# Kernel tuning notes

Measured on AMD Instinct MI355X. Metric: run time of the kernel, lower is better.

The kernel has to match this reference:

```python
import jax, jax.numpy as jnp
import numpy as np

D = 128      # state_dim
ED = 20      # edge_dim (RBF basis size)
R = 3        # num message/update rounds
G = 3        # gated equivariant blocks
CUT = 5.0    # cutoff
N = 10000    # nodes
E = 160000   # edges
B = 500      # molecules
HRO = 64     # readout hidden


def setup_inputs() -> dict:
    key = jax.random.key(0)
    ks = jax.random.split(key, 40)
    sc = 0.05

    def nrm(k, shape):
        return jax.random.normal(k, shape, dtype=jnp.float32) * sc

    inp = {
        "h": jax.random.normal(ks[0], (N, 5), dtype=jnp.float32),
        "pos": jax.random.normal(ks[1], (N, 3), dtype=jnp.float32),
        "edge_index": jax.random.randint(ks[2], (2, E), 0, N),
        "batch": jnp.sort(jax.random.randint(ks[3], (N,), 0, B)),
        # node embedding Linear(5, D)
        "emb_w": nrm(ks[4], (5, D)), "emb_b": nrm(ks[5], (D,)),
        # per-round message params (stacked over rounds)
        "msg_phi_w1": nrm(ks[6], (R, D, D)), "msg_phi_b1": nrm(ks[7], (R, D)),
        "msg_phi_w2": nrm(ks[8], (R, D, 3 * D)), "msg_phi_b2": nrm(ks[9], (R, 3 * D)),
        "msg_filt_w": nrm(ks[10], (R, ED, 3 * D)), "msg_filt_b": nrm(ks[11], (R, 3 * D)),
        # per-round update params
        "upd_U": nrm(ks[12], (R, D, D)), "upd_V": nrm(ks[13], (R, D, D)),
        "upd_w1": nrm(ks[14], (R, 2 * D, D)), "upd_b1": nrm(ks[15], (R, D)),
        "upd_w2": nrm(ks[16], (R, D, 3 * D)), "upd_b2": nrm(ks[17], (R, 3 * D)),
        # gated equivariant blocks
        "geb_wv1": nrm(ks[18], (G, D, D)), "geb_wv2": nrm(ks[19], (G, D, D)),
        "geb_w1": nrm(ks[20], (G, 2 * D, D)), "geb_b1": nrm(ks[21], (G, D)),
        "geb_w2": nrm(ks[22], (G, D, 2 * D)), "geb_b2": nrm(ks[23], (G, 2 * D)),
        # invariant readout MLP
        "ro_w1": nrm(ks[24], (D, HRO)), "ro_b1": nrm(ks[25], (HRO,)),
        "ro_w2": nrm(ks[26], (HRO, 1)), "ro_b2": nrm(ks[27], (1,)),
    }
    return inp


def _safe_norm(x, axis):
    return jnp.sqrt(jnp.sum(x * x, axis=axis) + 1e-8)


def reference(h, pos, edge_index, batch,
              emb_w, emb_b,
              msg_phi_w1, msg_phi_b1, msg_phi_w2, msg_phi_b2,
              msg_filt_w, msg_filt_b,
              upd_U, upd_V, upd_w1, upd_b1, upd_w2, upd_b2,
              geb_wv1, geb_wv2, geb_w1, geb_b1, geb_w2, geb_b2,
              ro_w1, ro_b1, ro_w2, ro_b2):
    n_nodes = h.shape[0]
    row, col = edge_index[0], edge_index[1]
    # edge vectors: r_ij = pos[col] - pos[row]
    r_ij = pos[col] - pos[row]                                   # [E,3]
    d = jnp.clip(jnp.linalg.norm(r_ij, axis=1, keepdims=True), 1e-6, None)  # [E,1]
    unit = r_ij / d                                              # [E,3]
    # sinc radial basis + cosine cutoff
    freqs = jnp.arange(1, ED + 1, dtype=h.dtype)
    rbf = jnp.sin(freqs * jnp.pi * d / CUT) / d                  # [E,ED]
    fcut = 0.5 * (jnp.cos(jnp.pi * d / CUT) + 1.0) * (d < CUT)   # [E,1]

    s = h @ emb_w + emb_b                                        # [N,D]
    v = jnp.zeros((n_nodes, D, 3), dtype=h.dtype)                # [N,D,3]

    for r in range(R):
        # --- PaiNNMessage ---
        phi = jax.nn.silu(s @ msg_phi_w1[r] + msg_phi_b1[r]) @ msg_phi_w2[r] + msg_phi_b2[r]  # [N,3D]
        filt = (rbf @ msg_filt_w[r] + msg_filt_b[r]) * fcut      # [E,3D]
        x = phi[col] * filt                                      # gather + modulate  [E,3D]
        xs, xvv, xvw = jnp.split(x, 3, axis=-1)                  # each [E,D]
        ds = jax.ops.segment_sum(xs, row, num_segments=n_nodes)  # [N,D]
        dv_e = xvv[:, :, None] * v[col] + xvw[:, :, None] * unit[:, None, :]  # [E,D,3]
        dv = jax.ops.segment_sum(dv_e, row, num_segments=n_nodes)             # [N,D,3]
        s = s + ds
        v = v + dv
        # --- PaiNNUpdate ---
        Uv = jnp.einsum('ndc,de->nec', v, upd_U[r])              # [N,D,3]
        Vv = jnp.einsum('ndc,de->nec', v, upd_V[r])              # [N,D,3]
        Vn = _safe_norm(Vv, axis=-1)                             # [N,D]
        a = jax.nn.silu(jnp.concatenate([s, Vn], axis=-1) @ upd_w1[r] + upd_b1[r]) @ upd_w2[r] + upd_b2[r]
        a_ss, a_sv, a_vv = jnp.split(a, 3, axis=-1)
        s = s + a_ss + a_sv * jnp.sum(Uv * Vv, axis=-1)
        v = v + a_vv[:, :, None] * Uv

    # --- GatedEquivariantBlocks ---
    for g in range(G):
        v1 = jnp.einsum('ndc,de->nec', v, geb_wv1[g])
        v2 = jnp.einsum('ndc,de->nec', v, geb_wv2[g])
        n2 = _safe_norm(v2, axis=-1)                             # [N,D]
        a = jax.nn.silu(jnp.concatenate([s, n2], axis=-1) @ geb_w1[g] + geb_b1[g]) @ geb_w2[g] + geb_b2[g]
        s_new, gate = jnp.split(a, 2, axis=-1)
        s = s_new
        v = gate[:, :, None] * v1

    # --- InvariantReadout + molwise scatter ---
    out = jax.nn.silu(s @ ro_w1 + ro_b1) @ ro_w2 + ro_b2         # [N,1]
    molwise = jax.ops.segment_sum(out, batch, num_segments=B)    # [B,1]
    return molwise.squeeze(-1)
```

## Files before the change

### kernel.cpp

```cpp
#include <hip/hip_runtime.h>

typedef __attribute__((ext_vector_type(4))) float f32x4;
typedef __attribute__((ext_vector_type(8))) short short8;

#define D 128
#define D3 384
#define SLD 256
#define EDIM 20
#define NR 3
#define NG 3
#define CUTOFF 5.0f
#define NNODES 10000
#define NEDGES 160000
#define NMOL 500
#define HROH 64
#define PI_F 3.14159265358979323846f

#define FBIAS 1
#define FSILU 2

static __device__ __forceinline__ float silu_f(float x) {
    return x / (1.0f + expf(-x));
}

static __device__ __forceinline__ ushort f2bf(float x) {
    uint u = __float_as_uint(x);
    uint r = (u + 0x7fffu + ((u >> 16) & 1u)) >> 16;
    return (ushort)r;
}
static __device__ __forceinline__ float bf2f(ushort h) {
    return __uint_as_float((uint)h << 16);
}

#define TLR 64
#define TLC 64
#define KC 32
#define APAD 40
#define BPAD 36

template <bool TWO>
__global__ __launch_bounds__(256) void gemm_t(
    const float* __restrict__ A, int lda, int zsA,
    const float* __restrict__ WA, const float* __restrict__ WB, int ldw,
    const float* __restrict__ bias,
    float* __restrict__ CA, float* __restrict__ CB, int ldc, int zsC,
    int N, int K, int flags)
{
    int coord, sel;
    if (TWO) { coord = blockIdx.z >> 1; sel = blockIdx.z & 1; }
    else     { coord = blockIdx.z;      sel = 0; }
    const float* W = (TWO && sel) ? WB : WA;
    float* C = ((TWO && sel) ? CB : CA) + (size_t)coord * zsC;
    A += (size_t)coord * zsA;

    const int n0 = blockIdx.x * TLR;
    const int m0 = blockIdx.y * TLC;
    __shared__ ushort Ah[TLR * APAD], Al[TLR * APAD];
    __shared__ ushort Bh[TLC * BPAD], Bl[TLC * BPAD];
    const int tid = threadIdx.x;
    const int arow = tid & 63;
    const int akq = (tid >> 6) * 4;
    const bool aok = (n0 + arow) < N;
    const float* Ar = A + (size_t)(n0 + arow) * lda;
    const int bk = tid >> 4;
    const int bm = (tid & 15) * 4;
    const float* Wp = W + m0 + bm;
    const int lane = tid & 63;
    const int wrow = (tid >> 6) * 16;
    const int fr = lane & 15;
    const int kg = lane >> 4;
    const ushort* aph = Ah + (wrow + fr) * APAD + kg * 8;
    const ushort* apl = Al + (wrow + fr) * APAD + kg * 8;

    f32x4 acc[4];
    #pragma unroll
    for (int t = 0; t < 4; ++t) acc[t] = (f32x4){0.f, 0.f, 0.f, 0.f};

    for (int k0 = 0; k0 < K; k0 += KC) {
        #pragma unroll
        for (int half = 0; half < 2; ++half) {
            int kk = akq + half * 16;
            float4 v = aok ? *(const float4*)(Ar + k0 + kk)
                           : make_float4(0.f, 0.f, 0.f, 0.f);
            ushort h0 = f2bf(v.x), h1 = f2bf(v.y), h2 = f2bf(v.z), h3 = f2bf(v.w);
            ushort l0 = f2bf(v.x - bf2f(h0)), l1 = f2bf(v.y - bf2f(h1));
            ushort l2 = f2bf(v.z - bf2f(h2)), l3 = f2bf(v.w - bf2f(h3));
            uint2 ph, pl;
            ph.x = (uint)h0 | ((uint)h1 << 16); ph.y = (uint)h2 | ((uint)h3 << 16);
            pl.x = (uint)l0 | ((uint)l1 << 16); pl.y = (uint)l2 | ((uint)l3 << 16);
            *(uint2*)(Ah + arow * APAD + kk) = ph;
            *(uint2*)(Al + arow * APAD + kk) = pl;
        }
        #pragma unroll
        for (int half = 0; half < 2; ++half) {
            int kk = bk + half * 16;
            float4 v = *(const float4*)(Wp + (size_t)(k0 + kk) * ldw);
            float vv[4] = {v.x, v.y, v.z, v.w};
            #pragma unroll
            for (int i = 0; i < 4; ++i) {
                ushort hh = f2bf(vv[i]);
                ushort ll = f2bf(vv[i] - bf2f(hh));
                Bh[(bm + i) * BPAD + kk] = hh;
                Bl[(bm + i) * BPAD + kk] = ll;
            }
        }
        __syncthreads();
        short8 ah = *(const short8*)aph;
        short8 al = *(const short8*)apl;
        #pragma unroll
        for (int t = 0; t < 4; ++t) {
            const ushort* bp = Bh + (t * 16 + fr) * BPAD + kg * 8;
            const ushort* bq = Bl + (t * 16 + fr) * BPAD + kg * 8;
            short8 bh, bl;
            ((uint2*)&bh)[0] = *(const uint2*)bp;
            ((uint2*)&bh)[1] = *(const uint2*)(bp + 4);
            ((uint2*)&bl)[0] = *(const uint2*)bq;
            ((uint2*)&bl)[1] = *(const uint2*)(bq + 4);
            acc[t] = __builtin_amdgcn_mfma_f32_16x16x32_bf16(ah, bh, acc[t], 0, 0, 0);
            acc[t] = __builtin_amdgcn_mfma_f32_16x16x32_bf16(al, bh, acc[t], 0, 0, 0);
            acc[t] = __builtin_amdgcn_mfma_f32_16x16x32_bf16(ah, bl, acc[t], 0, 0, 0);
        }
        __syncthreads();
    }
    #pragma unroll
    for (int t = 0; t < 4; ++t) {
        #pragma unroll
        for (int r = 0; r < 4; ++r) {
            int n = n0 + wrow + kg * 4 + r;
            if (n < N) {
                int m = m0 + t * 16 + fr;
                float val = acc[t][r];
                float* cp = C + (size_t)n * ldc + m;
                if (flags & FBIAS) val += bias[m];
                if (flags & FSILU) val = silu_f(val);
                *cp = val;
            }
        }
    }
}

__global__ __launch_bounds__(256) void emb_k(
    const float* __restrict__ h, const float* __restrict__ w,
    const float* __restrict__ b, float* __restrict__ s, int total)
{
    int i = blockIdx.x * 256 + threadIdx.x;
    if (i >= total) return;
    int n = i >> 7, d = i & 127;
    float acc = b[d];
    #pragma unroll
    for (int k = 0; k < 5; ++k) acc = fmaf(h[n * 5 + k], w[k * D + d], acc);
    s[(size_t)n * SLD + d] = acc;
}

__global__ __launch_bounds__(256) void hist_k(const int* __restrict__ ei,
                                              int* __restrict__ cnt, int E)
{
    int e = blockIdx.x * 256 + threadIdx.x;
    if (e < E) atomicAdd(&cnt[ei[e]], 1);
}

__global__ __launch_bounds__(256) void scan_k(const int* __restrict__ cnt,
                                              int* __restrict__ offs, int n)
{
    __shared__ int tmp[256];
    __shared__ int carry;
    if (threadIdx.x == 0) carry = 0;
    __syncthreads();
    for (int base = 0; base < n; base += 256) {
        int i = base + threadIdx.x;
        int v = (i < n) ? cnt[i] : 0;
        tmp[threadIdx.x] = v;
        __syncthreads();
        for (int off = 1; off < 256; off <<= 1) {
            int add = (threadIdx.x >= off) ? tmp[threadIdx.x - off] : 0;
            __syncthreads();
            tmp[threadIdx.x] += add;
            __syncthreads();
        }
        if (i < n) offs[i + 1] = carry + tmp[threadIdx.x];
        __syncthreads();
        if (threadIdx.x == 255) carry += tmp[255];
        __syncthreads();
    }
    if (threadIdx.x == 0) offs[0] = 0;
}

__global__ __launch_bounds__(256) void initnext_k(const int* __restrict__ offs,
                                                  int* __restrict__ next, int n)
{
    int i = blockIdx.x * 256 + threadIdx.x;
    if (i < n) next[i] = offs[i];
}

__global__ __launch_bounds__(256) void edge_pre_k(
    const int* __restrict__ ei, const float* __restrict__ pos,
    int* __restrict__ next, float* __restrict__ rbf_s,
    float* __restrict__ uf_s, int* __restrict__ col_s, int E)
{
    int e = blockIdx.x * 256 + threadIdx.x;
    if (e >= E) return;
    int r = ei[e], c = ei[E + e];
    float dx = pos[c * 3 + 0] - pos[r * 3 + 0];
    float dy = pos[c * 3 + 1] - pos[r * 3 + 1];
    float dz = pos[c * 3 + 2] - pos[r * 3 + 2];
    float dist = sqrtf(dx * dx + dy * dy + dz * dz);
    float d = fmaxf(dist, 1e-6f);
    float inv = 1.0f / d;
    int p = atomicAdd(&next[r], 1);
    col_s[p] = c;
    uf_s[p * 4 + 0] = dx * inv;
    uf_s[p * 4 + 1] = dy * inv;
    uf_s[p * 4 + 2] = dz * inv;
    uf_s[p * 4 + 3] = (d < CUTOFF) ? 0.5f * (cosf(PI_F * d / CUTOFF) + 1.0f) : 0.0f;
    float w = PI_F * d / CUTOFF;
    #pragma unroll
    for (int k = 1; k <= EDIM; ++k)
        rbf_s[(size_t)p * EDIM + (k - 1)] = sinf((float)k * w) * inv;
}

#define MSG_NPB 4
__global__ __launch_bounds__(256) void message_csr_k(
    const int* __restrict__ offs, const int* __restrict__ col_s,
    const float* __restrict__ rbf_s, const float* __restrict__ uf_s,
    const float* __restrict__ P, const float* __restrict__ Vold,
    const float* __restrict__ Wf, const float* __restrict__ bf,
    float* __restrict__ S, float* __restrict__ Vnew, int N)
{
    const int sub = threadIdx.x >> 7;
    const int d = threadIdx.x & 127;
    float ws[EDIM], wvv[EDIM], wvw[EDIM];
    #pragma unroll
    for (int k = 0; k < EDIM; ++k) {
        ws[k]  = Wf[k * D3 + d];
        wvv[k] = Wf[k * D3 + D + d];
        wvw[k] = Wf[k * D3 + 2 * D + d];
    }
    const float bs = bf[d], bvv = bf[D + d], bvw = bf[2 * D + d];

    auto edge = [&](int j, float& ds, float& dvx, float& dvy, float& dvz) {
        float4 u4 = *(const float4*)(uf_s + (size_t)j * 4);
        int col = col_s[j];
        const float* rb = rbf_s + (size_t)j * EDIM;
        float4 r0 = *(const float4*)(rb);
        float4 r1 = *(const float4*)(rb + 4);
        float4 r2 = *(const float4*)(rb + 8);
        float4 r3 = *(const float4*)(rb + 12);
        float4 r4 = *(const float4*)(rb + 16);
        float rv[EDIM] = {r0.x, r0.y, r0.z, r0.w, r1.x, r1.y, r1.z, r1.w,
                          r2.x, r2.y, r2.z, r2.w, r3.x, r3.y, r3.z, r3.w,
                          r4.x, r4.y, r4.z, r4.w};
        float fs = bs, fvv = bvv, fvw = bvw;
        #pragma unroll
        for (int k = 0; k < EDIM; ++k) {
            fs  = fmaf(rv[k], ws[k], fs);
            fvv = fmaf(rv[k], wvv[k], fvv);
            fvw = fmaf(rv[k], wvw[k], fvw);
        }
        float fc = u4.w;
        const float* pc = P + (size_t)col * D3;
        const float* vc = Vold + (size_t)col * D3;
        float xs  = pc[d] * fs * fc;
        float xvv = pc[D + d] * fvv * fc;
        float xvw = pc[2 * D + d] * fvw * fc;
        ds += xs;
        dvx = fmaf(xvv, vc[d],         fmaf(xvw, u4.x, dvx));
        dvy = fmaf(xvv, vc[D + d],     fmaf(xvw, u4.y, dvy));
        dvz = fmaf(xvv, vc[2 * D + d], fmaf(xvw, u4.z, dvz));
    };

    for (int it = 0; it < MSG_NPB / 2; ++it) {
        int n = blockIdx.x * MSG_NPB + it * 2 + sub;
        if (n >= N) return;
        float ds0 = 0.f, dx0 = 0.f, dy0 = 0.f, dz0 = 0.f;
        float ds1 = 0.f, dx1 = 0.f, dy1 = 0.f, dz1 = 0.f;
        const int j0 = offs[n], j1 = offs[n + 1];
        int j = j0;
        for (; j + 2 <= j1; j += 2) {
            edge(j, ds0, dx0, dy0, dz0);
            edge(j + 1, ds1, dx1, dy1, dz1);
        }
        if (j < j1) edge(j, ds0, dx0, dy0, dz0);
        S[(size_t)n * SLD + d] += ds0 + ds1;
        const float* vo = Vold + (size_t)n * D3;
        float* vn = Vnew + (size_t)n * D3;
        vn[d]         = vo[d] + dx0 + dx1;
        vn[D + d]     = vo[D + d] + dy0 + dy1;
        vn[2 * D + d] = vo[2 * D + d] + dz0 + dz1;
    }
}

__global__ __launch_bounds__(256) void norm3_k(const float* __restrict__ V3,
                                               float* __restrict__ SX, int total)
{
    int i = blockIdx.x * 256 + threadIdx.x;
    if (i >= total) return;
    int n = i >> 7, d = i & 127;
    const float* b = V3 + (size_t)n * D3;
    float x = b[d], y = b[D + d], z = b[2 * D + d];
    SX[(size_t)n * SLD + D + d] = sqrtf(fmaf(x, x, fmaf(y, y, fmaf(z, z, 1e-8f))));
}

__global__ __launch_bounds__(256) void upd_apply_k(
    const float* __restrict__ U3, const float* __restrict__ V3,
    const float* __restrict__ P, float* __restrict__ s,
    float* __restrict__ v, int total)
{
    int i = blockIdx.x * 256 + threadIdx.x;
    if (i >= total) return;
    int n = i >> 7, d = i & 127;
    const float* u = U3 + (size_t)n * D3;
    const float* w = V3 + (size_t)n * D3;
    float ux = u[d], uy = u[D + d], uz = u[2 * D + d];
    float vx = w[d], vy = w[D + d], vz = w[2 * D + d];
    float dot = fmaf(ux, vx, fmaf(uy, vy, uz * vz));
    const float* a = P + (size_t)n * D3;
    s[(size_t)n * SLD + d] += a[d] + a[D + d] * dot;
    float avv = a[2 * D + d];
    float* vv = v + (size_t)n * D3;
    vv[d]         = fmaf(avv, ux, vv[d]);
    vv[D + d]     = fmaf(avv, uy, vv[D + d]);
    vv[2 * D + d] = fmaf(avv, uz, vv[2 * D + d]);
}

__global__ __launch_bounds__(256) void geb_apply_k(
    const float* __restrict__ P, const float* __restrict__ U3,
    float* __restrict__ s, float* __restrict__ v, int total)
{
    int i = blockIdx.x * 256 + threadIdx.x;
    if (i >= total) return;
    int n = i >> 7, d = i & 127;
    const float* a = P + (size_t)n * 2 * D;
    s[(size_t)n * SLD + d] = a[d];
    float g = a[D + d];
    const float* u = U3 + (size_t)n * D3;
    float* vv = v + (size_t)n * D3;
    vv[d]         = g * u[d];
    vv[D + d]     = g * u[D + d];
    vv[2 * D + d] = g * u[2 * D + d];
}

__global__ __launch_bounds__(256) void readout_k(
    const float* __restrict__ H2, const float* __restrict__ w2,
    const float* __restrict__ b2, const int* __restrict__ batch,
    float* __restrict__ out, int N)
{
    int n = blockIdx.x * 256 + threadIdx.x;
    if (n >= N) return;
    float acc = b2[0];
    const float* hrow = H2 + (size_t)n * HROH;
    #pragma unroll
    for (int k = 0; k < HROH; ++k) acc = fmaf(hrow[k], w2[k], acc);
    atomicAdd(out + batch[n], acc);
}


static inline void gemm(hipStream_t st, const float* A, int lda, int zsA,
                        const float* W, int ldw, const float* bias,
                        float* C, int ldc, int zsC,
                        int N, int K, int M, int flags, int Z = 1)
{
    dim3 g((N + TLR - 1) / TLR, M / TLC, Z);
    hipLaunchKernelGGL(HIP_KERNEL_NAME(gemm_t<false>), g, dim3(256), 0, st,
                       A, lda, zsA, W, nullptr, ldw, bias, C, nullptr, ldc, zsC,
                       N, K, flags);
}

static inline void gemm2(hipStream_t st, const float* A, int lda, int zsA,
                         const float* WA, const float* WB, int ldw,
                         float* CA, float* CB, int ldc, int zsC,
                         int N, int K, int M)
{
    dim3 g((N + TLR - 1) / TLR, M / TLC, 6);
    hipLaunchKernelGGL(HIP_KERNEL_NAME(gemm_t<true>), g, dim3(256), 0, st,
                       A, lda, zsA, WA, WB, ldw, nullptr, CA, CB, ldc, zsC,
                       N, K, 0);
}

extern "C" void kernel_launch(void* const* d_in, const int* in_sizes, int n_in,
                              void* d_out, int out_size, void* d_ws, size_t ws_size,
                              hipStream_t stream)
{
    const float* h          = (const float*)d_in[0];
    const float* pos        = (const float*)d_in[1];
    const int*   ei         = (const int*)d_in[2];
    const int*   batch      = (const int*)d_in[3];
    const float* emb_w      = (const float*)d_in[4];
    const float* emb_b      = (const float*)d_in[5];
    const float* msg_phi_w1 = (const float*)d_in[6];
    const float* msg_phi_b1 = (const float*)d_in[7];
    const float* msg_phi_w2 = (const float*)d_in[8];
    const float* msg_phi_b2 = (const float*)d_in[9];
    const float* msg_filt_w = (const float*)d_in[10];
    const float* msg_filt_b = (const float*)d_in[11];
    const float* upd_U      = (const float*)d_in[12];
    const float* upd_V      = (const float*)d_in[13];
    const float* upd_w1     = (const float*)d_in[14];
    const float* upd_b1     = (const float*)d_in[15];
    const float* upd_w2     = (const float*)d_in[16];
    const float* upd_b2     = (const float*)d_in[17];
    const float* geb_wv1    = (const float*)d_in[18];
    const float* geb_wv2    = (const float*)d_in[19];
    const float* geb_w1     = (const float*)d_in[20];
    const float* geb_b1     = (const float*)d_in[21];
    const float* geb_w2     = (const float*)d_in[22];
    const float* geb_b2     = (const float*)d_in[23];
    const float* ro_w1      = (const float*)d_in[24];
    const float* ro_b1      = (const float*)d_in[25];
    const float* ro_w2      = (const float*)d_in[26];
    const float* ro_b2      = (const float*)d_in[27];
    float* out = (float*)d_out;

    const int N = NNODES, E = NEDGES;

    char* p = (char*)d_ws;
    auto carve = [&](size_t bytes) {
        char* r = p;
        p += (bytes + 255) & ~(size_t)255;
        return r;
    };
    float* SX   = (float*)carve((size_t)N * SLD * 4);
    float* VA   = (float*)carve((size_t)N * D3 * 4);
    float* VB   = (float*)carve((size_t)N * D3 * 4);
    float* P_   = (float*)carve((size_t)N * D3 * 4);
    float* H    = (float*)carve((size_t)N * D * 4);
    float* H2   = (float*)carve((size_t)N * D * 4);
    float* V3   = (float*)carve((size_t)N * D3 * 4);
    float* RBFs = (float*)carve((size_t)E * EDIM * 4);
    float* UFs  = (float*)carve((size_t)E * 4 * 4);
    int*   COLs = (int*)carve((size_t)E * 4);
    int*   offs = (int*)carve((size_t)(N + 1) * 4);
    int*   nxt  = (int*)carve((size_t)N * 4);

    hipMemsetAsync(VA, 0, (size_t)N * D3 * 4, stream);
    hipLaunchKernelGGL(emb_k, dim3((N * D + 255) / 256), dim3(256), 0, stream,
                       h, emb_w, emb_b, SX, N * D);
    hipMemsetAsync(nxt, 0, (size_t)N * 4, stream);
    hipLaunchKernelGGL(hist_k, dim3((E + 255) / 256), dim3(256), 0, stream, ei, nxt, E);
    hipLaunchKernelGGL(scan_k, dim3(1), dim3(256), 0, stream, nxt, offs, N);
    hipLaunchKernelGGL(initnext_k, dim3((N + 255) / 256), dim3(256), 0, stream,
                       offs, nxt, N);
    hipLaunchKernelGGL(edge_pre_k, dim3((E + 255) / 256), dim3(256), 0, stream,
                       ei, pos, nxt, RBFs, UFs, COLs, E);

    float* Vc = VA;
    float* Vs = VB;

    for (int r = 0; r < NR; ++r) {
        gemm(stream, SX, SLD, 0, msg_phi_w1 + (size_t)r * D * D, D,
             msg_phi_b1 + (size_t)r * D, H, D, 0, N, D, D, FBIAS | FSILU);
        gemm(stream, H, D, 0, msg_phi_w2 + (size_t)r * D * D3, D3,
             msg_phi_b2 + (size_t)r * D3, P_, D3, 0, N, D, D3, FBIAS);
        hipLaunchKernelGGL(message_csr_k, dim3((N + MSG_NPB - 1) / MSG_NPB),
                           dim3(256), 0, stream,
                           offs, COLs, RBFs, UFs, P_, Vc,
                           msg_filt_w + (size_t)r * EDIM * D3,
                           msg_filt_b + (size_t)r * D3, SX, Vs, N);
        { float* t = Vc; Vc = Vs; Vs = t; }
        float* Uv = Vs;
        gemm2(stream, Vc, D3, D, upd_U + (size_t)r * D * D,
              upd_V + (size_t)r * D * D, D, Uv, V3, D3, D, N, D, D);
        hipLaunchKernelGGL(norm3_k, dim3((N * D + 255) / 256), dim3(256), 0, stream,
                           V3, SX, N * D);
        gemm(stream, SX, SLD, 0, upd_w1 + (size_t)r * 2 * D * D, D,
             upd_b1 + (size_t)r * D, H2, D, 0, N, 2 * D, D, FBIAS | FSILU);
        gemm(stream, H2, D, 0, upd_w2 + (size_t)r * D * D3, D3,
             upd_b2 + (size_t)r * D3, P_, D3, 0, N, D, D3, FBIAS);
        hipLaunchKernelGGL(upd_apply_k, dim3((N * D + 255) / 256), dim3(256), 0, stream,
                           Uv, V3, P_, SX, Vc, N * D);
    }

    for (int g = 0; g < NG; ++g) {
        float* Uv = Vs;
        gemm2(stream, Vc, D3, D, geb_wv1 + (size_t)g * D * D,
              geb_wv2 + (size_t)g * D * D, D, Uv, V3, D3, D, N, D, D);
        hipLaunchKernelGGL(norm3_k, dim3((N * D + 255) / 256), dim3(256), 0, stream,
                           V3, SX, N * D);
        gemm(stream, SX, SLD, 0, geb_w1 + (size_t)g * 2 * D * D, D,
             geb_b1 + (size_t)g * D, H2, D, 0, N, 2 * D, D, FBIAS | FSILU);
        gemm(stream, H2, D, 0, geb_w2 + (size_t)g * D * 2 * D, 2 * D,
             geb_b2 + (size_t)g * 2 * D, P_, 2 * D, 0, N, D, 2 * D, FBIAS);
        hipLaunchKernelGGL(geb_apply_k, dim3((N * D + 255) / 256), dim3(256), 0, stream,
                           P_, Uv, SX, Vc, N * D);
    }

    gemm(stream, SX, SLD, 0, ro_w1, HROH, ro_b1, H2, HROH, 0, N, D, HROH,
         FBIAS | FSILU);
    hipMemsetAsync(out, 0, (size_t)NMOL * 4, stream);
    hipLaunchKernelGGL(readout_k, dim3((N + 255) / 256), dim3(256), 0, stream,
                       H2, ro_w2, ro_b2, batch, out, N);
}
```

Baseline: 979.7 us.

## Fuse U/V vector GEMMs with norm and dot; gather bf16 P and V in messages

Replaces the batched two-weight GEMM plus separate norm kernel with a fused kernel. It computes Uv and Vv for all three components in one tile, writes the norm straight into the scalar buffer and optionally the U·V dot product. This drops the V3 intermediate and the norm3 launch. Separately, the message kernel now gathers bf16 copies of P and v instead of fp32. This halves the bytes moved in the edge-irregular gather, at the cost of extra bf16 shadow writes and reduced precision in the message inputs.

After: 936.4 us. 1.05x faster.

```diff
diff --git a/kernel.cpp b/kernel.cpp
--- a/kernel.cpp
+++ b/kernel.cpp
@@ -18,6 +18,7 @@
 
 #define FBIAS 1
 #define FSILU 2
+#define FBF16O 4
 
 static __device__ __forceinline__ float silu_f(float x) {
     return x / (1.0f + expf(-x));
@@ -38,21 +39,13 @@
 #define APAD 40
 #define BPAD 36
 
-template <bool TWO>
-__global__ __launch_bounds__(256) void gemm_t(
-    const float* __restrict__ A, int lda, int zsA,
-    const float* __restrict__ WA, const float* __restrict__ WB, int ldw,
+__global__ __launch_bounds__(256) void gemm_k(
+    const float* __restrict__ A, int lda,
+    const float* __restrict__ W, int ldw,
     const float* __restrict__ bias,
-    float* __restrict__ CA, float* __restrict__ CB, int ldc, int zsC,
+    float* __restrict__ C, ushort* __restrict__ Cbf, int ldc,
     int N, int K, int flags)
 {
-    int coord, sel;
-    if (TWO) { coord = blockIdx.z >> 1; sel = blockIdx.z & 1; }
-    else     { coord = blockIdx.z;      sel = 0; }
-    const float* W = (TWO && sel) ? WB : WA;
-    float* C = ((TWO && sel) ? CB : CA) + (size_t)coord * zsC;
-    A += (size_t)coord * zsA;
-
     const int n0 = blockIdx.x * TLR;
     const int m0 = blockIdx.y * TLC;
     __shared__ ushort Ah[TLR * APAD], Al[TLR * APAD];
@@ -130,10 +123,127 @@
             if (n < N) {
                 int m = m0 + t * 16 + fr;
                 float val = acc[t][r];
-                float* cp = C + (size_t)n * ldc + m;
                 if (flags & FBIAS) val += bias[m];
                 if (flags & FSILU) val = silu_f(val);
-                *cp = val;
+                if (flags & FBF16O) Cbf[(size_t)n * ldc + m] = f2bf(val);
+                else                C[(size_t)n * ldc + m] = val;
+            }
+        }
+    }
+}
+
+template <bool WITHDOT>
+__global__ __launch_bounds__(256) void uvn_k(
+    const float* __restrict__ A,
+    const float* __restrict__ WU, const float* __restrict__ WV,
+    float* __restrict__ Uv,
+    float* __restrict__ DOT,
+    float* __restrict__ SX, int N)
+{
+    const int n0 = blockIdx.x * 64;
+    const int m0 = blockIdx.y * 64;
+    __shared__ ushort Ah[3][64 * APAD], Al[3][64 * APAD];
+    __shared__ ushort Bh[2][64 * BPAD], Bl[2][64 * BPAD];
+    const int tid = threadIdx.x;
+    const int arow = tid & 63;
+    const int akq = (tid >> 6) * 4;
+    const bool aok = (n0 + arow) < N;
+    const float* Ar = A + (size_t)(n0 + arow) * D3;
+    const int bk = tid >> 4;
+    const int bm = (tid & 15) * 4;
+    const int lane = tid & 63;
+    const int wrow = (tid >> 6) * 16;
+    const int fr = lane & 15;
+    const int kg = lane >> 4;
+
+    f32x4 acc[3][2][4];
+    #pragma unroll
+    for (int c = 0; c < 3; ++c)
+        #pragma unroll
+        for (int s = 0; s < 2; ++s)
+            #pragma unroll
+            for (int t = 0; t < 4; ++t) acc[c][s][t] = (f32x4){0.f, 0.f, 0.f, 0.f};
+
+    for (int k0 = 0; k0 < D; k0 += KC) {
+        #pragma unroll
+        for (int c = 0; c < 3; ++c) {
+            #pragma unroll
+            for (int half = 0; half < 2; ++half) {
+                int kk = akq + half * 16;
+                float4 v = aok ? *(const float4*)(Ar + c * D + k0 + kk)
+                               : make_float4(0.f, 0.f, 0.f, 0.f);
+                ushort h0 = f2bf(v.x), h1 = f2bf(v.y), h2 = f2bf(v.z), h3 = f2bf(v.w);
+                ushort l0 = f2bf(v.x - bf2f(h0)), l1 = f2bf(v.y - bf2f(h1));
+                ushort l2 = f2bf(v.z - bf2f(h2)), l3 = f2bf(v.w - bf2f(h3));
+                uint2 ph, pl;
+                ph.x = (uint)h0 | ((uint)h1 << 16); ph.y = (uint)h2 | ((uint)h3 << 16);
+                pl.x = (uint)l0 | ((uint)l1 << 16); pl.y = (uint)l2 | ((uint)l3 << 16);
+                *(uint2*)(&Ah[c][arow * APAD + kk]) = ph;
+                *(uint2*)(&Al[c][arow * APAD + kk]) = pl;
+            }
+        }
+        #pragma unroll
+        for (int s = 0; s < 2; ++s) {
+            const float* W = s ? WV : WU;
+            #pragma unroll
+            for (int half = 0; half < 2; ++half) {
+                int kk = bk + half * 16;
+                float4 v = *(const float4*)(W + (size_t)(k0 + kk) * D + m0 + bm);
+                float vv[4] = {v.x, v.y, v.z, v.w};
+                #pragma unroll
+                for (int i = 0; i < 4; ++i) {
+                    ushort hh = f2bf(vv[i]);
+                    ushort ll = f2bf(vv[i] - bf2f(hh));
+                    Bh[s][(bm + i) * BPAD + kk] = hh;
+                    Bl[s][(bm + i) * BPAD + kk] = ll;
+                }
+            }
+        }
+        __syncthreads();
+        short8 ah[3], al[3];
+        #pragma unroll
+        for (int c = 0; c < 3; ++c) {
+            ah[c] = *(const short8*)(&Ah[c][(wrow + fr) * APAD + kg * 8]);
+            al[c] = *(const short8*)(&Al[c][(wrow + fr) * APAD + kg * 8]);
+        }
+        #pragma unroll
+        for (int t = 0; t < 4; ++t) {
+            #pragma unroll
+            for (int s = 0; s < 2; ++s) {
+                const ushort* bp = &Bh[s][(t * 16 + fr) * BPAD + kg * 8];
+                const ushort* bq = &Bl[s][(t * 16 + fr) * BPAD + kg * 8];
+                short8 bh, bl;
+                ((uint2*)&bh)[0] = *(const uint2*)bp;
+                ((uint2*)&bh)[1] = *(const uint2*)(bp + 4);
+                ((uint2*)&bl)[0] = *(const uint2*)bq;
+                ((uint2*)&bl)[1] = *(const uint2*)(bq + 4);
+                #pragma unroll
+                for (int c = 0; c < 3; ++c) {
+                    acc[c][s][t] = __builtin_amdgcn_mfma_f32_16x16x32_bf16(ah[c], bh, acc[c][s][t], 0, 0, 0);
+                    acc[c][s][t] = __builtin_amdgcn_mfma_f32_16x16x32_bf16(al[c], bh, acc[c][s][t], 0, 0, 0);
+                    acc[c][s][t] = __builtin_amdgcn_mfma_f32_16x16x32_bf16(ah[c], bl, acc[c][s][t], 0, 0, 0);
+                }
+            }
+        }
+        __syncthreads();
+    }
+    #pragma unroll
+    for (int t = 0; t < 4; ++t) {
+        #pragma unroll
+        for (int r = 0; r < 4; ++r) {
+            int n = n0 + wrow + kg * 4 + r;
+            if (n < N) {
+                int m = m0 + t * 16 + fr;
+                float ux = acc[0][0][t][r], uy = acc[1][0][t][r], uz = acc[2][0][t][r];
+                float vx = acc[0][1][t][r], vy = acc[1][1][t][r], vz = acc[2][1][t][r];
+                float* up = Uv + (size_t)n * D3 + m;
+                up[0]     = ux;
+                up[D]     = uy;
+                up[2 * D] = uz;
+                SX[(size_t)n * SLD + D + m] =
+                    sqrtf(fmaf(vx, vx, fmaf(vy, vy, fmaf(vz, vz, 1e-8f))));
+                if (WITHDOT)
+                    DOT[(size_t)n * D + m] = fmaf(ux, vx, fmaf(uy, vy, uz * vz));
             }
         }
     }
@@ -222,9 +332,11 @@
 __global__ __launch_bounds__(256) void message_csr_k(
     const int* __restrict__ offs, const int* __restrict__ col_s,
     const float* __restrict__ rbf_s, const float* __restrict__ uf_s,
-    const float* __restrict__ P, const float* __restrict__ Vold,
+    const ushort* __restrict__ Pbf, const float* __restrict__ Vold,
+    const ushort* __restrict__ VbfOld,
     const float* __restrict__ Wf, const float* __restrict__ bf,
-    float* __restrict__ S, float* __restrict__ Vnew, int N)
+    float* __restrict__ S, float* __restrict__ Vnew,
+    ushort* __restrict__ VbfNew, int N)
 {
     const int sub = threadIdx.x >> 7;
     const int d = threadIdx.x & 127;
@@ -257,15 +369,15 @@
             fvw = fmaf(rv[k], wvw[k], fvw);
         }
         float fc = u4.w;
-        const float* pc = P + (size_t)col * D3;
-        const float* vc = Vold + (size_t)col * D3;
-        float xs  = pc[d] * fs * fc;
-        float xvv = pc[D + d] * fvv * fc;
-        float xvw = pc[2 * D + d] * fvw * fc;
+        const ushort* pc = Pbf + (size_t)col * D3;
+        const ushort* vc = VbfOld + (size_t)col * D3;
+        float xs  = bf2f(pc[d]) * fs * fc;
+        float xvv = bf2f(pc[D + d]) * fvv * fc;
+        float xvw = bf2f(pc[2 * D + d]) * fvw * fc;
         ds += xs;
-        dvx = fmaf(xvv, vc[d],         fmaf(xvw, u4.x, dvx));
-        dvy = fmaf(xvv, vc[D + d],     fmaf(xvw, u4.y, dvy));
-        dvz = fmaf(xvv, vc[2 * D + d], fmaf(xvw, u4.z, dvz));
+        dvx = fmaf(xvv, bf2f(vc[d]),         fmaf(xvw, u4.x, dvx));
+        dvy = fmaf(xvv, bf2f(vc[D + d]),     fmaf(xvw, u4.y, dvy));
+        dvz = fmaf(xvv, bf2f(vc[2 * D + d]), fmaf(xvw, u4.z, dvz));
     };
 
     for (int it = 0; it < MSG_NPB / 2; ++it) {
@@ -283,43 +395,37 @@
         S[(size_t)n * SLD + d] += ds0 + ds1;
         const float* vo = Vold + (size_t)n * D3;
         float* vn = Vnew + (size_t)n * D3;
-        vn[d]         = vo[d] + dx0 + dx1;
-        vn[D + d]     = vo[D + d] + dy0 + dy1;
-        vn[2 * D + d] = vo[2 * D + d] + dz0 + dz1;
-    }
-}
-
-__global__ __launch_bounds__(256) void norm3_k(const float* __restrict__ V3,
-                                               float* __restrict__ SX, int total)
-{
-    int i = blockIdx.x * 256 + threadIdx.x;
-    if (i >= total) return;
-    int n = i >> 7, d = i & 127;
-    const float* b = V3 + (size_t)n * D3;
-    float x = b[d], y = b[D + d], z = b[2 * D + d];
-    SX[(size_t)n * SLD + D + d] = sqrtf(fmaf(x, x, fmaf(y, y, fmaf(z, z, 1e-8f))));
+        ushort* vb = VbfNew + (size_t)n * D3;
+        float nx = vo[d] + dx0 + dx1;
+        float ny = vo[D + d] + dy0 + dy1;
+        float nz = vo[2 * D + d] + dz0 + dz1;
+        vn[d] = nx;         vb[d] = f2bf(nx);
+        vn[D + d] = ny;     vb[D + d] = f2bf(ny);
+        vn[2 * D + d] = nz; vb[2 * D + d] = f2bf(nz);
+    }
 }
 
 __global__ __launch_bounds__(256) void upd_apply_k(
-    const float* __restrict__ U3, const float* __restrict__ V3,
+    const float* __restrict__ U3, const float* __restrict__ DOT,
     const float* __restrict__ P, float* __restrict__ s,
-    float* __restrict__ v, int total)
+    float* __restrict__ v, ushort* __restrict__ vbf, int total)
 {
     int i = blockIdx.x * 256 + threadIdx.x;
     if (i >= total) return;
     int n = i >> 7, d = i & 127;
     const float* u = U3 + (size_t)n * D3;
-    const float* w = V3 + (size_t)n * D3;
     float ux = u[d], uy = u[D + d], uz = u[2 * D + d];
-    float vx = w[d], vy = w[D + d], vz = w[2 * D + d];
-    float dot = fmaf(ux, vx, fmaf(uy, vy, uz * vz));
     const float* a = P + (size_t)n * D3;
-    s[(size_t)n * SLD + d] += a[d] + a[D + d] * dot;
+    s[(size_t)n * SLD + d] += a[d] + a[D + d] * DOT[i];
     float avv = a[2 * D + d];
     float* vv = v + (size_t)n * D3;
-    vv[d]         = fmaf(avv, ux, vv[d]);
-    vv[D + d]     = fmaf(avv, uy, vv[D + d]);
-    vv[2 * D + d] = fmaf(avv, uz, vv[2 * D + d]);
+    ushort* vb = vbf + (size_t)n * D3;
+    float nx = fmaf(avv, ux, vv[d]);
+    float ny = fmaf(avv, uy, vv[D + d]);
+    float nz = fmaf(avv, uz, vv[2 * D + d]);
+    vv[d] = nx;         vb[d] = f2bf(nx);
+    vv[D + d] = ny;     vb[D + d] = f2bf(ny);
+    vv[2 * D + d] = nz; vb[2 * D + d] = f2bf(nz);
 }
 
 __global__ __launch_bounds__(256) void geb_apply_k(
@@ -354,26 +460,14 @@
 }
 
 
-static inline void gemm(hipStream_t st, const float* A, int lda, int zsA,
+static inline void gemm(hipStream_t st, const float* A, int lda,
                         const float* W, int ldw, const float* bias,
-                        float* C, int ldc, int zsC,
-                        int N, int K, int M, int flags, int Z = 1)
-{
-    dim3 g((N + TLR - 1) / TLR, M / TLC, Z);
-    hipLaunchKernelGGL(HIP_KERNEL_NAME(gemm_t<false>), g, dim3(256), 0, st,
-                       A, lda, zsA, W, nullptr, ldw, bias, C, nullptr, ldc, zsC,
-                       N, K, flags);
-}
-
-static inline void gemm2(hipStream_t st, const float* A, int lda, int zsA,
-                         const float* WA, const float* WB, int ldw,
-                         float* CA, float* CB, int ldc, int zsC,
-                         int N, int K, int M)
-{
-    dim3 g((N + TLR - 1) / TLR, M / TLC, 6);
-    hipLaunchKernelGGL(HIP_KERNEL_NAME(gemm_t<true>), g, dim3(256), 0, st,
-                       A, lda, zsA, WA, WB, ldw, nullptr, CA, CB, ldc, zsC,
-                       N, K, 0);
+                        float* C, ushort* Cbf, int ldc,
+                        int N, int K, int M, int flags)
+{
+    dim3 g((N + TLR - 1) / TLR, M / TLC, 1);
+    hipLaunchKernelGGL(gemm_k, g, dim3(256), 0, st,
+                       A, lda, W, ldw, bias, C, Cbf, ldc, N, K, flags);
 }
 
 extern "C" void kernel_launch(void* const* d_in, const int* in_sizes, int n_in,
@@ -418,20 +512,23 @@
         p += (bytes + 255) & ~(size_t)255;
         return r;
     };
-    float* SX   = (float*)carve((size_t)N * SLD * 4);
-    float* VA   = (float*)carve((size_t)N * D3 * 4);
-    float* VB   = (float*)carve((size_t)N * D3 * 4);
-    float* P_   = (float*)carve((size_t)N * D3 * 4);
-    float* H    = (float*)carve((size_t)N * D * 4);
-    float* H2   = (float*)carve((size_t)N * D * 4);
-    float* V3   = (float*)carve((size_t)N * D3 * 4);
-    float* RBFs = (float*)carve((size_t)E * EDIM * 4);
-    float* UFs  = (float*)carve((size_t)E * 4 * 4);
-    int*   COLs = (int*)carve((size_t)E * 4);
-    int*   offs = (int*)carve((size_t)(N + 1) * 4);
-    int*   nxt  = (int*)carve((size_t)N * 4);
+    float*  SX   = (float*)carve((size_t)N * SLD * 4);
+    float*  VA   = (float*)carve((size_t)N * D3 * 4);
+    float*  VB   = (float*)carve((size_t)N * D3 * 4);
+    float*  P_   = (float*)carve((size_t)N * D3 * 4);
+    ushort* Pbf  = (ushort*)P_;
+    ushort* VBFa = (ushort*)carve((size_t)N * D3 * 2);
+    ushort* VBFb = (ushort*)carve((size_t)N * D3 * 2);
+    float*  H    = (float*)carve((size_t)N * D * 4);
+    float*  H2   = (float*)carve((size_t)N * D * 4);
+    float*  RBFs = (float*)carve((size_t)E * EDIM * 4);
+    float*  UFs  = (float*)carve((size_t)E * 4 * 4);
+    int*    COLs = (int*)carve((size_t)E * 4);
+    int*    offs = (int*)carve((size_t)(N + 1) * 4);
+    int*    nxt  = (int*)carve((size_t)N * 4);
 
     hipMemsetAsync(VA, 0, (size_t)N * D3 * 4, stream);
+    hipMemsetAsync(VBFa, 0, (size_t)N * D3 * 2, stream);
     hipLaunchKernelGGL(emb_k, dim3((N * D + 255) / 256), dim3(256), 0, stream,
                        h, emb_w, emb_b, SX, N * D);
     hipMemsetAsync(nxt, 0, (size_t)N * 4, stream);
@@ -442,48 +539,50 @@
     hipLaunchKernelGGL(edge_pre_k, dim3((E + 255) / 256), dim3(256), 0, stream,
                        ei, pos, nxt, RBFs, UFs, COLs, E);
 
-    float* Vc = VA;
-    float* Vs = VB;
+    float*  Vc = VA;   ushort* VbfC = VBFa;
+    float*  Vs = VB;   ushort* VbfS = VBFb;
 
     for (int r = 0; r < NR; ++r) {
-        gemm(stream, SX, SLD, 0, msg_phi_w1 + (size_t)r * D * D, D,
-             msg_phi_b1 + (size_t)r * D, H, D, 0, N, D, D, FBIAS | FSILU);
-        gemm(stream, H, D, 0, msg_phi_w2 + (size_t)r * D * D3, D3,
-             msg_phi_b2 + (size_t)r * D3, P_, D3, 0, N, D, D3, FBIAS);
+        gemm(stream, SX, SLD, msg_phi_w1 + (size_t)r * D * D, D,
+             msg_phi_b1 + (size_t)r * D, H, nullptr, D, N, D, D, FBIAS | FSILU);
+        gemm(stream, H, D, msg_phi_w2 + (size_t)r * D * D3, D3,
+             msg_phi_b2 + (size_t)r * D3, nullptr, Pbf, D3, N, D, D3,
+             FBIAS | FBF16O);
         hipLaunchKernelGGL(message_csr_k, dim3((N + MSG_NPB - 1) / MSG_NPB),
                            dim3(256), 0, stream,
-                           offs, COLs, RBFs, UFs, P_, Vc,
+                           offs, COLs, RBFs, UFs, Pbf, Vc, VbfC,
                            msg_filt_w + (size_t)r * EDIM * D3,
-                           msg_filt_b + (size_t)r * D3, SX, Vs, N);
+                           msg_filt_b + (size_t)r * D3, SX, Vs, VbfS, N);
         { float* t = Vc; Vc = Vs; Vs = t; }
+        { ushort* t = VbfC; VbfC = VbfS; VbfS = t; }
         float* Uv = Vs;
-        gemm2(stream, Vc, D3, D, upd_U + (size_t)r * D * D,
-              upd_V + (size_t)r * D * D, D, Uv, V3, D3, D, N, D, D);
-        hipLaunchKernelGGL(norm3_k, dim3((N * D + 255) / 256), dim3(256), 0, stream,
-                           V3, SX, N * D);
-        gemm(stream, SX, SLD, 0, upd_w1 + (size_t)r * 2 * D * D, D,
-             upd_b1 + (size_t)r * D, H2, D, 0, N, 2 * D, D, FBIAS | FSILU);
-        gemm(stream, H2, D, 0, upd_w2 + (size_t)r * D * D3, D3,
-             upd_b2 + (size_t)r * D3, P_, D3, 0, N, D, D3, FBIAS);
-        hipLaunchKernelGGL(upd_apply_k, dim3((N * D + 255) / 256), dim3(256), 0, stream,
-                           Uv, V3, P_, SX, Vc, N * D);
+        hipLaunchKernelGGL(HIP_KERNEL_NAME(uvn_k<true>),
+                           dim3((N + 63) / 64, 2), dim3(256), 0, stream,
+                           Vc, upd_U + (size_t)r * D * D,
+                           upd_V + (size_t)r * D * D, Uv, H, SX, N);
+        gemm(stream, SX, SLD, upd_w1 + (size_t)r * 2 * D * D, D,
+             upd_b1 + (size_t)r * D, H2, nullptr, D, N, 2 * D, D, FBIAS | FSILU);
+        gemm(stream, H2, D, upd_w2 + (size_t)r * D * D3, D3,
+             upd_b2 + (size_t)r * D3, P_, nullptr, D3, N, D, D3, FBIAS);
+        hipLaunchKernelGGL(upd_apply_k, dim3((N * D + 255) / 256), dim3(256), 0,
+                           stream, Uv, H, P_, SX, Vc, VbfC, N * D);
     }
 
     for (int g = 0; g < NG; ++g) {
         float* Uv = Vs;
-        gemm2(stream, Vc, D3, D, geb_wv1 + (size_t)g * D * D,
-              geb_wv2 + (size_t)g * D * D, D, Uv, V3, D3, D, N, D, D);
-        hipLaunchKernelGGL(norm3_k, dim3((N * D + 255) / 256), dim3(256), 0, stream,
-                           V3, SX, N * D);
-        gemm(stream, SX, SLD, 0, geb_w1 + (size_t)g * 2 * D * D, D,
-             geb_b1 + (size_t)g * D, H2, D, 0, N, 2 * D, D, FBIAS | FSILU);
-        gemm(stream, H2, D, 0, geb_w2 + (size_t)g * D * 2 * D, 2 * D,
-             geb_b2 + (size_t)g * 2 * D, P_, 2 * D, 0, N, D, 2 * D, FBIAS);
-        hipLaunchKernelGGL(geb_apply_k, dim3((N * D + 255) / 256), dim3(256), 0, stream,
-                           P_, Uv, SX, Vc, N * D);
-    }
-
-    gemm(stream, SX, SLD, 0, ro_w1, HROH, ro_b1, H2, HROH, 0, N, D, HROH,
+        hipLaunchKernelGGL(HIP_KERNEL_NAME(uvn_k<false>),
+                           dim3((N + 63) / 64, 2), dim3(256), 0, stream,
+                           Vc, geb_wv1 + (size_t)g * D * D,
+                           geb_wv2 + (size_t)g * D * D, Uv, nullptr, SX, N);
+        gemm(stream, SX, SLD, geb_w1 + (size_t)g * 2 * D * D, D,
+             geb_b1 + (size_t)g * D, H2, nullptr, D, N, 2 * D, D, FBIAS | FSILU);
+        gemm(stream, H2, D, geb_w2 + (size_t)g * D * 2 * D, 2 * D,
+             geb_b2 + (size_t)g * 2 * D, P_, nullptr, 2 * D, N, D, 2 * D, FBIAS);
+        hipLaunchKernelGGL(geb_apply_k, dim3((N * D + 255) / 256), dim3(256), 0,
+                           stream, P_, Uv, SX, Vc, N * D);
+    }
+
+    gemm(stream, SX, SLD, ro_w1, HROH, ro_b1, H2, nullptr, HROH, N, D, HROH,
          FBIAS | FSILU);
     hipMemsetAsync(out, 0, (size_t)NMOL * 4, stream);
     hipLaunchKernelGGL(readout_k, dim3((N + 255) / 256), dim3(256), 0, stream,
```
